# Performance work log

Hardware: AMD Instinct MI355X
Metric: run time of the kernel (lower is better)

## Reference

```python
import jax, jax.numpy as jnp
import numpy as np

N = 500_000
EPS_IN = 1e-6   # point-in-box tolerance (matches mmcv diff_iou_rotated)
EPS_IOU = 1e-8


def _box2corners(box):
    # box [N,7]: (x,y,z,w,l,h,alpha) -> BEV rectangle corners [N,4,2]
    x, y = box[:, 0], box[:, 1]
    w, l, a = box[:, 3], box[:, 4], box[:, 6]
    tx = jnp.array([0.5, -0.5, -0.5, 0.5], dtype=box.dtype)
    ty = jnp.array([0.5, 0.5, -0.5, -0.5], dtype=box.dtype)
    x4 = tx[None, :] * w[:, None]
    y4 = ty[None, :] * l[:, None]
    c, s = jnp.cos(a)[:, None], jnp.sin(a)[:, None]
    cx = x4 * c - y4 * s + x[:, None]
    cy = x4 * s + y4 * c + y[:, None]
    return jnp.stack([cx, cy], axis=-1)


def _cross2(a, b):
    return a[..., 0] * b[..., 1] - a[..., 1] * b[..., 0]


def _edge_intersections(c1, c2):
    # all 4x4 edge-pair segment intersections -> pts [N,16,2], mask [N,16]
    p1 = c1[:, :, None, :]                         # [N,4,1,2]
    p2 = jnp.roll(c1, -1, axis=1)[:, :, None, :]
    q1 = c2[:, None, :, :]                         # [N,1,4,2]
    q2 = jnp.roll(c2, -1, axis=1)[:, None, :, :]
    r = p2 - p1
    s = q2 - q1
    den = _cross2(r, s)
    den_safe = jnp.where(den == 0, 1.0, den)
    t = _cross2(q1 - p1, s) / den_safe
    u = _cross2(q1 - p1, r) / den_safe
    mask = (den != 0) & (t > 0) & (t < 1) & (u > 0) & (u < 1)
    pts = jnp.where(mask[..., None], p1 + t[..., None] * r, 0.0)
    n = c1.shape[0]
    return pts.reshape(n, 16, 2), mask.reshape(n, 16)


def _points_in_box(pts, corners):
    # pts [N,4,2] inside rotated rect given by corners [N,4,2]
    a = corners[:, 0:1]
    b = corners[:, 1:2]
    d = corners[:, 3:4]
    ab, ad, ap = b - a, d - a, pts - a
    pab = jnp.sum(ap * ab, -1) / jnp.sum(ab * ab, -1)
    pad_ = jnp.sum(ap * ad, -1) / jnp.sum(ad * ad, -1)
    return (pab > -EPS_IN) & (pab < 1 + EPS_IN) & (pad_ > -EPS_IN) & (pad_ < 1 + EPS_IN)


def _polygon_area(verts, mask):
    # verts [N,24,2], mask [N,24]: sort valid vertices CCW around their mean,
    # close the polygon, shoelace area. Invalid slots set to first valid vertex
    # so they contribute zero cross terms.
    maskf = mask.astype(verts.dtype)
    nv = jnp.maximum(jnp.sum(maskf, axis=1, keepdims=True), 1.0)
    mean = jnp.sum(verts * maskf[..., None], axis=1, keepdims=True) / nv[..., None]
    cen = verts - mean
    ang = jnp.where(mask, jnp.arctan2(cen[..., 1], cen[..., 0]), 1e9)
    order = jnp.argsort(ang, axis=1)
    s = jnp.take_along_axis(cen, order[..., None], axis=1)
    m = jnp.take_along_axis(mask, order, axis=1)
    v0 = s[:, 0:1, :]  # first valid vertex (valid slots sort first)
    s = jnp.where(m[..., None], s, v0)
    s_next = jnp.roll(s, -1, axis=1)
    return 0.5 * jnp.abs(jnp.sum(_cross2(s, s_next), axis=1))


def _rotated_iou_3d(pred, target):
    c1 = _box2corners(pred)
    c2 = _box2corners(target)
    inter_pts, inter_mask = _edge_intersections(c1, c2)
    in12 = _points_in_box(c1, c2)
    in21 = _points_in_box(c2, c1)
    verts = jnp.concatenate([c1, c2, inter_pts], axis=1)      # [N,24,2]
    mask = jnp.concatenate([in12, in21, inter_mask], axis=1)  # [N,24]
    inter_area = _polygon_area(verts, mask)
    zt = jnp.minimum(pred[:, 2] + 0.5 * pred[:, 5], target[:, 2] + 0.5 * target[:, 5])
    zb = jnp.maximum(pred[:, 2] - 0.5 * pred[:, 5], target[:, 2] - 0.5 * target[:, 5])
    inter_vol = inter_area * jnp.clip(zt - zb, 0.0)
    v1 = pred[:, 3] * pred[:, 4] * pred[:, 5]
    v2 = target[:, 3] * target[:, 4] * target[:, 5]
    return inter_vol / (v1 + v2 - inter_vol + EPS_IOU)


def setup_inputs() -> dict:
    key = jax.random.key(0)
    k1, k2, k3, k4 = jax.random.split(key, 4)
    centers = jax.random.uniform(k1, (N, 3), jnp.float32, -50.0, 50.0)
    dims = jax.random.uniform(k2, (N, 3), jnp.float32, 1.0, 4.0)
    alpha = jax.random.uniform(k3, (N, 1), jnp.float32, -np.pi, np.pi)
    target = jnp.concatenate([centers, dims, alpha], axis=1)
    noise_scale = jnp.array([0.5, 0.5, 0.3, 0.2, 0.2, 0.2, 0.1], jnp.float32)
    pred = target + jax.random.normal(k4, (N, 7), jnp.float32) * noise_scale
    pred = pred.at[:, 3:6].set(jnp.maximum(pred[:, 3:6], 0.1))  # keep dims positive
    return {"pred": pred, "target": target}


def reference(pred, target):
    # RotatedIoU3DLoss(mode='iou', reduction='mean', loss_weight=1.0)
    return 1.0 * jnp.mean(1.0 - _rotated_iou_3d(pred, target))
```

## Files before the change

### kernel.cpp

```cpp
#include <hip/hip_runtime.h>
#include <math.h>

#define EPS_IOU 1e-8f
#define IPB 512
#define NF (IPB * 7)

__device__ __forceinline__ float slab_dt(float sx, float sy,
                                         float rdx, float rdy,
                                         float hx, float hy)
{
    float tx1 = (-hx - sx) * rdx, tx2 = (hx - sx) * rdx;
    float ty1 = (-hy - sy) * rdy, ty2 = (hy - sy) * rdy;
    float t0 = fmaxf(fmaxf(fminf(tx1, tx2), fminf(ty1, ty2)), 0.0f);
    float t1 = fminf(fminf(fmaxf(tx1, tx2), fmaxf(ty1, ty2)), 1.0f);
    return fmaxf(t1 - t0, 0.0f);
}

__device__ __forceinline__ float one_loss(const float* __restrict__ P,
                                          const float* __restrict__ T)
{
    float px = P[0], py = P[1], pz = P[2], pw = P[3], pl = P[4], ph = P[5], pa = P[6];
    float qx = T[0], qy = T[1], qz = T[2], qw = T[3], ql = T[4], qh = T[5], qa = T[6];

    float hpx = 0.5f * pw, hpy = 0.5f * pl;
    float hqx = 0.5f * qw, hqy = 0.5f * ql;

    float ca, sa, cb, sb;
    __sincosf(pa, &sa, &ca);
    __sincosf(qa, &sb, &cb);
    float ct = ca * cb + sa * sb;
    float st = sb * ca - sa * cb;

    float dxw = qx - px, dyw = qy - py;
    float cx_ =  ca * dxw + sa * dyw;
    float cy_ = -sa * dxw + ca * dyw;

    float ux = ct * hqx, uy = st * hqx;
    float vx = -st * hqy, vy = ct * hqy;

    float r2ux = __builtin_amdgcn_rcpf(2.0f * ux);
    float r2uy = __builtin_amdgcn_rcpf(2.0f * uy);
    float r2vx = __builtin_amdgcn_rcpf(2.0f * vx);
    float r2vy = __builtin_amdgcn_rcpf(2.0f * vy);

    float upx = ux + vx, upy = uy + vy;
    float umx = ux - vx, umy = uy - vy;
    float dq0 = slab_dt(cx_ + upx, cy_ + upy, -r2ux, -r2uy, hpx, hpy);
    float dq1 = slab_dt(cx_ - umx, cy_ - umy, -r2vx, -r2vy, hpx, hpy);
    float dq2 = slab_dt(cx_ - upx, cy_ - upy,  r2ux,  r2uy, hpx, hpy);
    float dq3 = slab_dt(cx_ + umx, cy_ + umy,  r2vx,  r2vy, hpx, hpy);

    float Cu = cx_ * uy - cy_ * ux;
    float Cv = cx_ * vy - cy_ * vx;
    float W2 = 2.0f * (hqx * hqy);
    float Cu2 = 2.0f * Cu, Cv2 = 2.0f * Cv;
    float area2 = dq0 * (W2 - Cu2) + dq1 * (W2 - Cv2)
                + dq2 * (W2 + Cu2) + dq3 * (W2 + Cv2);

    float u2x = ct * hpx, u2y = -st * hpx;
    float v2x = st * hpy, v2y = ct * hpy;
    float c2x = -(ct * cx_ + st * cy_);
    float c2y = st * cx_ - ct * cy_;

    float r2u2x = __builtin_amdgcn_rcpf(2.0f * u2x);
    float r2u2y = __builtin_amdgcn_rcpf(2.0f * u2y);
    float r2v2x = __builtin_amdgcn_rcpf(2.0f * v2x);
    float r2v2y = __builtin_amdgcn_rcpf(2.0f * v2y);

    float up2x = u2x + v2x, up2y = u2y + v2y;
    float um2x = u2x - v2x, um2y = u2y - v2y;
    float dtp = slab_dt(c2x + up2x, c2y + up2y, -r2u2x, -r2u2y, hqx, hqy)
              + slab_dt(c2x - um2x, c2y - um2y, -r2v2x, -r2v2y, hqx, hqy)
              + slab_dt(c2x - up2x, c2y - up2y,  r2u2x,  r2u2y, hqx, hqy)
              + slab_dt(c2x + um2x, c2y + um2y,  r2v2x,  r2v2y, hqx, hqy);
    area2 += dtp * (2.0f * (hpx * hpy));

    float inter_area = 0.5f * fabsf(area2);

    float zt = fminf(pz + 0.5f * ph, qz + 0.5f * qh);
    float zb = fmaxf(pz - 0.5f * ph, qz - 0.5f * qh);
    float hz = fmaxf(zt - zb, 0.0f);
    float inter_vol = inter_area * hz;
    float v1 = pw * pl * ph;
    float v2 = qw * ql * qh;
    float iou = inter_vol * __builtin_amdgcn_rcpf(v1 + v2 - inter_vol + EPS_IOU);
    return 1.0f - iou;
}

__global__ __launch_bounds__(256) void iou_main_kernel(
    const float* __restrict__ pred,
    const float* __restrict__ target,
    float* __restrict__ partial,
    int n, float invN)
{
    __shared__ float sP[NF];
    __shared__ float sT[NF];

    const int base = blockIdx.x * IPB;
    const int rem = min(IPB, n - base);
    const int nf = rem * 7;

    const float4* gp = (const float4*)(pred + (size_t)base * 7);
    const float4* gt = (const float4*)(target + (size_t)base * 7);
    float4* lp = (float4*)sP;
    float4* lt = (float4*)sT;
    for (int k = threadIdx.x; k * 4 < nf; k += 256) {
        if (k * 4 + 3 < nf) {
            lp[k] = gp[k];
            lt[k] = gt[k];
        } else {
            for (int c = k * 4; c < nf; ++c) {
                sP[c] = pred[(size_t)base * 7 + c];
                sT[c] = target[(size_t)base * 7 + c];
            }
        }
    }
    __syncthreads();

    float loss = 0.0f;
#pragma unroll
    for (int it = 0; it < 2; ++it) {
        int j = threadIdx.x + it * 256;
        if (j < rem) loss += one_loss(sP + 7 * j, sT + 7 * j) * invN;
    }

#pragma unroll
    for (int off = 32; off > 0; off >>= 1)
        loss += __shfl_down(loss, off, 64);
    __shared__ float wsum[4];
    int lane = threadIdx.x & 63;
    int wid = threadIdx.x >> 6;
    if (lane == 0) wsum[wid] = loss;
    __syncthreads();
    if (threadIdx.x == 0)
        partial[blockIdx.x] = wsum[0] + wsum[1] + wsum[2] + wsum[3];
}

__global__ __launch_bounds__(256) void iou_reduce_kernel(
    const float* __restrict__ partial, float* __restrict__ out, int g)
{
    float s = 0.0f;
    for (int k = threadIdx.x; k < g; k += 256) s += partial[k];
#pragma unroll
    for (int off = 32; off > 0; off >>= 1)
        s += __shfl_down(s, off, 64);
    __shared__ float wsum[4];
    int lane = threadIdx.x & 63;
    int wid = threadIdx.x >> 6;
    if (lane == 0) wsum[wid] = s;
    __syncthreads();
    if (threadIdx.x == 0)
        out[0] = wsum[0] + wsum[1] + wsum[2] + wsum[3];
}

extern "C" void kernel_launch(void* const* d_in, const int* in_sizes, int n_in,
                              void* d_out, int out_size, void* d_ws, size_t ws_size,
                              hipStream_t stream) {
    const float* pred = (const float*)d_in[0];
    const float* target = (const float*)d_in[1];
    float* out = (float*)d_out;
    float* partial = (float*)d_ws;
    int n = in_sizes[0] / 7;

    int grid = (n + IPB - 1) / IPB;
    iou_main_kernel<<<grid, 256, 0, stream>>>(pred, target, partial, n,
                                              1.0f / (float)n);
    iou_reduce_kernel<<<1, 256, 0, stream>>>(partial, out, grid);
}
```

Measured before the change: 76.46 us.

## Drop LDS staging and load box fields directly per thread

Removes the shared-memory staging of pred/target and the block barrier. Each thread now handles one box pair and reads its 7 fields straight from global memory, with twice as many blocks. The slab test also drops the factor of 2 by using 1/u reciprocals with a clamp of 2. The mean scaling moves into the final reduce, and sincos is split into separate sin/cos. The risk is stride-7 uncoalesced global loads replacing the vectorized float4 copies.

```diff
diff --git a/kernel.cpp b/kernel.cpp
--- a/kernel.cpp
+++ b/kernel.cpp
@@ -2,8 +2,6 @@
 #include <math.h>
 
 #define EPS_IOU 1e-8f
-#define IPB 512
-#define NF (IPB * 7)
 
 __device__ __forceinline__ float slab_dt(float sx, float sy,
                                          float rdx, float rdy,
@@ -12,22 +10,20 @@
     float tx1 = (-hx - sx) * rdx, tx2 = (hx - sx) * rdx;
     float ty1 = (-hy - sy) * rdy, ty2 = (hy - sy) * rdy;
     float t0 = fmaxf(fmaxf(fminf(tx1, tx2), fminf(ty1, ty2)), 0.0f);
-    float t1 = fminf(fminf(fmaxf(tx1, tx2), fmaxf(ty1, ty2)), 1.0f);
+    float t1 = fminf(fminf(fmaxf(tx1, tx2), fmaxf(ty1, ty2)), 2.0f);
     return fmaxf(t1 - t0, 0.0f);
 }
 
-__device__ __forceinline__ float one_loss(const float* __restrict__ P,
-                                          const float* __restrict__ T)
+__device__ __forceinline__ float one_loss(float px, float py, float pz,
+                                          float pw, float pl, float ph, float pa,
+                                          float qx, float qy, float qz,
+                                          float qw, float ql, float qh, float qa)
 {
-    float px = P[0], py = P[1], pz = P[2], pw = P[3], pl = P[4], ph = P[5], pa = P[6];
-    float qx = T[0], qy = T[1], qz = T[2], qw = T[3], ql = T[4], qh = T[5], qa = T[6];
-
     float hpx = 0.5f * pw, hpy = 0.5f * pl;
     float hqx = 0.5f * qw, hqy = 0.5f * ql;
 
-    float ca, sa, cb, sb;
-    __sincosf(pa, &sa, &ca);
-    __sincosf(qa, &sb, &cb);
+    float sa = __sinf(pa), ca = __cosf(pa);
+    float sb = __sinf(qa), cb = __cosf(qa);
     float ct = ca * cb + sa * sb;
     float st = sb * ca - sa * cb;
 
@@ -38,42 +34,41 @@
     float ux = ct * hqx, uy = st * hqx;
     float vx = -st * hqy, vy = ct * hqy;
 
-    float r2ux = __builtin_amdgcn_rcpf(2.0f * ux);
-    float r2uy = __builtin_amdgcn_rcpf(2.0f * uy);
-    float r2vx = __builtin_amdgcn_rcpf(2.0f * vx);
-    float r2vy = __builtin_amdgcn_rcpf(2.0f * vy);
+    float rux = __builtin_amdgcn_rcpf(ux);
+    float ruy = __builtin_amdgcn_rcpf(uy);
+    float rvx = __builtin_amdgcn_rcpf(vx);
+    float rvy = __builtin_amdgcn_rcpf(vy);
 
     float upx = ux + vx, upy = uy + vy;
     float umx = ux - vx, umy = uy - vy;
-    float dq0 = slab_dt(cx_ + upx, cy_ + upy, -r2ux, -r2uy, hpx, hpy);
-    float dq1 = slab_dt(cx_ - umx, cy_ - umy, -r2vx, -r2vy, hpx, hpy);
-    float dq2 = slab_dt(cx_ - upx, cy_ - upy,  r2ux,  r2uy, hpx, hpy);
-    float dq3 = slab_dt(cx_ + umx, cy_ + umy,  r2vx,  r2vy, hpx, hpy);
+    float dq0 = slab_dt(cx_ + upx, cy_ + upy, -rux, -ruy, hpx, hpy);
+    float dq1 = slab_dt(cx_ - umx, cy_ - umy, -rvx, -rvy, hpx, hpy);
+    float dq2 = slab_dt(cx_ - upx, cy_ - upy,  rux,  ruy, hpx, hpy);
+    float dq3 = slab_dt(cx_ + umx, cy_ + umy,  rvx,  rvy, hpx, hpy);
 
     float Cu = cx_ * uy - cy_ * ux;
     float Cv = cx_ * vy - cy_ * vx;
-    float W2 = 2.0f * (hqx * hqy);
-    float Cu2 = 2.0f * Cu, Cv2 = 2.0f * Cv;
-    float area2 = dq0 * (W2 - Cu2) + dq1 * (W2 - Cv2)
-                + dq2 * (W2 + Cu2) + dq3 * (W2 + Cv2);
+    float W = hqx * hqy;
+    float area2 = dq0 * (W - Cu) + dq1 * (W - Cv)
+                + dq2 * (W + Cu) + dq3 * (W + Cv);
 
     float u2x = ct * hpx, u2y = -st * hpx;
     float v2x = st * hpy, v2y = ct * hpy;
     float c2x = -(ct * cx_ + st * cy_);
     float c2y = st * cx_ - ct * cy_;
 
-    float r2u2x = __builtin_amdgcn_rcpf(2.0f * u2x);
-    float r2u2y = __builtin_amdgcn_rcpf(2.0f * u2y);
-    float r2v2x = __builtin_amdgcn_rcpf(2.0f * v2x);
-    float r2v2y = __builtin_amdgcn_rcpf(2.0f * v2y);
+    float ru2x = __builtin_amdgcn_rcpf(u2x);
+    float ru2y = __builtin_amdgcn_rcpf(u2y);
+    float rv2x = __builtin_amdgcn_rcpf(v2x);
+    float rv2y = __builtin_amdgcn_rcpf(v2y);
 
     float up2x = u2x + v2x, up2y = u2y + v2y;
     float um2x = u2x - v2x, um2y = u2y - v2y;
-    float dtp = slab_dt(c2x + up2x, c2y + up2y, -r2u2x, -r2u2y, hqx, hqy)
-              + slab_dt(c2x - um2x, c2y - um2y, -r2v2x, -r2v2y, hqx, hqy)
-              + slab_dt(c2x - up2x, c2y - up2y,  r2u2x,  r2u2y, hqx, hqy)
-              + slab_dt(c2x + um2x, c2y + um2y,  r2v2x,  r2v2y, hqx, hqy);
-    area2 += dtp * (2.0f * (hpx * hpy));
+    float dtp = slab_dt(c2x + up2x, c2y + up2y, -ru2x, -ru2y, hqx, hqy)
+              + slab_dt(c2x - um2x, c2y - um2y, -rv2x, -rv2y, hqx, hqy)
+              + slab_dt(c2x - up2x, c2y - up2y,  ru2x,  ru2y, hqx, hqy)
+              + slab_dt(c2x + um2x, c2y + um2y,  rv2x,  rv2y, hqx, hqy);
+    area2 += dtp * (hpx * hpy);
 
     float inter_area = 0.5f * fabsf(area2);
 
@@ -91,37 +86,15 @@
     const float* __restrict__ pred,
     const float* __restrict__ target,
     float* __restrict__ partial,
-    int n, float invN)
+    int n)
 {
-    __shared__ float sP[NF];
-    __shared__ float sT[NF];
-
-    const int base = blockIdx.x * IPB;
-    const int rem = min(IPB, n - base);
-    const int nf = rem * 7;
-
-    const float4* gp = (const float4*)(pred + (size_t)base * 7);
-    const float4* gt = (const float4*)(target + (size_t)base * 7);
-    float4* lp = (float4*)sP;
-    float4* lt = (float4*)sT;
-    for (int k = threadIdx.x; k * 4 < nf; k += 256) {
-        if (k * 4 + 3 < nf) {
-            lp[k] = gp[k];
-            lt[k] = gt[k];
-        } else {
-            for (int c = k * 4; c < nf; ++c) {
-                sP[c] = pred[(size_t)base * 7 + c];
-                sT[c] = target[(size_t)base * 7 + c];
-            }
-        }
-    }
-    __syncthreads();
-
+    int i = blockIdx.x * 256 + threadIdx.x;
     float loss = 0.0f;
-#pragma unroll
-    for (int it = 0; it < 2; ++it) {
-        int j = threadIdx.x + it * 256;
-        if (j < rem) loss += one_loss(sP + 7 * j, sT + 7 * j) * invN;
+    if (i < n) {
+        const float* P = pred + 7 * (size_t)i;
+        const float* T = target + 7 * (size_t)i;
+        loss = one_loss(P[0], P[1], P[2], P[3], P[4], P[5], P[6],
+                        T[0], T[1], T[2], T[3], T[4], T[5], T[6]);
     }
 
 #pragma unroll
@@ -137,7 +110,8 @@
 }
 
 __global__ __launch_bounds__(256) void iou_reduce_kernel(
-    const float* __restrict__ partial, float* __restrict__ out, int g)
+    const float* __restrict__ partial, float* __restrict__ out,
+    int g, float invN)
 {
     float s = 0.0f;
     for (int k = threadIdx.x; k < g; k += 256) s += partial[k];
@@ -150,7 +124,7 @@
     if (lane == 0) wsum[wid] = s;
     __syncthreads();
     if (threadIdx.x == 0)
-        out[0] = wsum[0] + wsum[1] + wsum[2] + wsum[3];
+        out[0] = (wsum[0] + wsum[1] + wsum[2] + wsum[3]) * invN;
 }
 
 extern "C" void kernel_launch(void* const* d_in, const int* in_sizes, int n_in,
@@ -162,8 +136,7 @@
     float* partial = (float*)d_ws;
     int n = in_sizes[0] / 7;
 
-    int grid = (n + IPB - 1) / IPB;
-    iou_main_kernel<<<grid, 256, 0, stream>>>(pred, target, partial, n,
-                                              1.0f / (float)n);
-    iou_reduce_kernel<<<1, 256, 0, stream>>>(partial, out, grid);
+    int grid = (n + 255) / 256;
+    iou_main_kernel<<<grid, 256, 0, stream>>>(pred, target, partial, n);
+    iou_reduce_kernel<<<1, 256, 0, stream>>>(partial, out, grid, 1.0f / (float)n);
 }
```

New measurement: 75.41 us. Within noise of the previous version (-1.4%).
